# Kernel optimization log

Measured on AMD Instinct MI355X. Metric: run time of the kernel, lower is better.

## Reference

```python
import jax, jax.numpy as jnp
import numpy as np

C = 128          # inchannel
CH = C // 2      # projected channels
N_, D_, H_, W_ = 2, 16, 16, 16


def setup_inputs() -> dict:
    key = jax.random.key(0)
    kx, kq, kk, kv, kp = jax.random.split(key, 5)
    s_in = 1.0 / np.sqrt(C)
    s_mid = 1.0 / np.sqrt(CH)
    return {
        "x": jax.random.normal(kx, (N_, C, D_, H_, W_), dtype=jnp.float32),
        "Wq": jax.random.normal(kq, (CH, C), dtype=jnp.float32) * s_in,
        "Wk": jax.random.normal(kk, (CH, C), dtype=jnp.float32) * s_in,
        "Wv": jax.random.normal(kv, (CH, C), dtype=jnp.float32) * s_in,
        "Wpost": jax.random.normal(kp, (C, CH), dtype=jnp.float32) * s_mid,
    }


def reference(x, Wq, Wk, Wv, Wpost):
    n, c_in, d, h, w = x.shape
    npos = d * h * w
    xf = x.reshape(n, c_in, npos)                     # (n, C, N)
    # 1x1x1 conv3d (no bias) == channel-mixing matmul
    q = jnp.einsum('oc,ncx->nox', Wq, xf)             # (n, CH, N)
    k = jnp.einsum('oc,ncx->nox', Wk, xf)             # (n, CH, N)
    v = jnp.einsum('oc,ncx->nox', Wv, xf)             # (n, CH, N)
    # atten_map[b,i,j] = sum_c k[b,c,i] * q[b,c,j], softmax over j (dim=2)
    scores = jnp.einsum('nci,ncj->nij', k, q)         # (n, N, N)
    attn = jax.nn.softmax(scores, axis=2)
    # val @ attn: out[b,c,j] = sum_i v[b,c,i] * attn[b,i,j]
    agg = jnp.einsum('nci,nij->ncj', v, attn)         # (n, CH, N)
    post = jnp.einsum('oc,ncx->nox', Wpost, agg)      # (n, C, N)
    return post.reshape(n, c_in, d, h, w) + x
```

## Files before the change

kernel.cpp:

```cpp
#include <hip/hip_runtime.h>
#include <math.h>

#define NB   2
#define CIN  128
#define CH   64
#define NPOS 4096

typedef __attribute__((ext_vector_type(8))) short s16x8;
typedef __attribute__((ext_vector_type(4))) float f32x4;

__device__ __forceinline__ unsigned int bfrne(float f) {
    unsigned int u = __float_as_uint(f);
    return (u + 0x7FFFu + ((u >> 16) & 1u)) >> 16;
}
__device__ __forceinline__ unsigned int pk_rne(float lo, float hi) {
    return bfrne(lo) | (bfrne(hi) << 16);
}
__device__ __forceinline__ unsigned int pk_fast(float lo, float hi) {
    unsigned int a = (__float_as_uint(lo) + 0x8000u) >> 16;
    unsigned int b = (__float_as_uint(hi) + 0x8000u) & 0xFFFF0000u;
    return a | b;
}
__device__ __forceinline__ float bf2f(unsigned short h) {
    return __uint_as_float(((unsigned int)h) << 16);
}

#define XTS 132
__global__ __launch_bounds__(256) void qkv_kernel(
    const float* __restrict__ x,
    const float* __restrict__ Wq, const float* __restrict__ Wk,
    const float* __restrict__ Wv,
    unsigned short* __restrict__ kT, unsigned short* __restrict__ qT,
    unsigned short* __restrict__ vbs)
{
    __shared__ __align__(16) float xT[16 * XTS];
    const int b  = blockIdx.y;
    const int p0 = blockIdx.x * 16;
    const int tid = threadIdx.x;

    #pragma unroll
    for (int it = 0; it < 2; ++it) {
        int idx = it * 256 + tid;
        int c = idx >> 2, p4 = (idx & 3) * 4;
        float4 g = *(const float4*)&x[((size_t)b * CIN + c) * NPOS + p0 + p4];
        xT[(p4 + 0) * XTS + c] = g.x;
        xT[(p4 + 1) * XTS + c] = g.y;
        xT[(p4 + 2) * XTS + c] = g.z;
        xT[(p4 + 3) * XTS + c] = g.w;
    }
    __syncthreads();

    const int w = tid >> 6, l = tid & 63, lm = l & 15, lq = l >> 4;
    const int p = p0 + lm;

    s16x8 Bhi[4], Blo[4];
    #pragma unroll
    for (int ck = 0; ck < 4; ++ck) {
        const float* xr = &xT[lm * XTS + ck * 32 + lq * 8];
        union { unsigned int u[4]; s16x8 v; } chv, clv;
        #pragma unroll
        for (int j = 0; j < 4; ++j) {
            float x0 = xr[2 * j], x1 = xr[2 * j + 1];
            unsigned int h0 = bfrne(x0), h1 = bfrne(x1);
            chv.u[j] = h0 | (h1 << 16);
            clv.u[j] = pk_rne(x0 - __uint_as_float(h0 << 16),
                              x1 - __uint_as_float(h1 << 16));
        }
        Bhi[ck] = chv.v; Blo[ck] = clv.v;
    }

    #pragma unroll
    for (int t3 = 0; t3 < 3; ++t3) {
        const int tile = w * 3 + t3;
        const int mat = tile >> 2, o0 = (tile & 3) * 16;
        const float* __restrict__ W = (mat == 0) ? Wq : (mat == 1) ? Wk : Wv;
        f32x4 acc = {0.f, 0.f, 0.f, 0.f};
        #pragma unroll
        for (int ck = 0; ck < 4; ++ck) {
            const float* wp = W + (o0 + lm) * CIN + ck * 32 + lq * 8;
            union { unsigned int u[4]; s16x8 v; } ca;
            #pragma unroll
            for (int j = 0; j < 4; ++j) ca.u[j] = pk_rne(wp[2*j], wp[2*j+1]);
            acc = __builtin_amdgcn_mfma_f32_16x16x32_bf16(ca.v, Bhi[ck], acc, 0,0,0);
            acc = __builtin_amdgcn_mfma_f32_16x16x32_bf16(ca.v, Blo[ck], acc, 0,0,0);
        }
        if (mat < 2) {
            unsigned short* dst = (mat == 0) ? qT : kT;
            uint2 st = make_uint2(pk_rne(acc[0], acc[1]), pk_rne(acc[2], acc[3]));
            *(uint2*)&dst[((size_t)b * NPOS + p) * CH + o0 + lq * 4] = st;
        } else {
            #pragma unroll
            for (int r = 0; r < 4; ++r)
                vbs[((size_t)b * CH + o0 + lq * 4 + r) * NPOS + p] =
                    (unsigned short)bfrne(acc[r]);
        }
    }
}

__global__ __launch_bounds__(256, 4) void stats_kernel(
    const unsigned short* __restrict__ kT,
    const unsigned short* __restrict__ qT,
    float* __restrict__ lpart)
{
    __shared__ __align__(16) unsigned short qbuf[2][4096];
    const int b  = blockIdx.z;
    const int jq = blockIdx.y;
    const int i0 = blockIdx.x * 128;
    const int tid = threadIdx.x;
    const int w = tid >> 6, l = tid & 63, lm = l & 15, lq = l >> 4;

    s16x8 a[2][2];
    #pragma unroll
    for (int s = 0; s < 2; ++s)
        #pragma unroll
        for (int kc = 0; kc < 2; ++kc)
            a[s][kc] = *(const s16x8*)&kT[
                ((size_t)b * NPOS + i0 + w * 32 + s * 16 + lm) * CH + kc * 32 + lq * 8];

    const unsigned short* qpt =
        qT + ((size_t)b * NPOS + jq * 512 + w * 16 + lm) * CH + lq * 8;
    s16x8 st0 = *(const s16x8*)(qpt);
    s16x8 st1 = *(const s16x8*)(qpt + 32);

    float rs[2][4] = {};
    for (int t = 0; t < 8; ++t) {
        const int buf = t & 1;
        *(s16x8*)&qbuf[buf][(2 * w + 0) * 512 + l * 8] = st0;
        *(s16x8*)&qbuf[buf][(2 * w + 1) * 512 + l * 8] = st1;
        if (t < 7) {
            const unsigned short* qn = qpt + (size_t)(t + 1) * 64 * CH;
            st0 = *(const s16x8*)(qn);
            st1 = *(const s16x8*)(qn + 32);
        }
        __syncthreads();
        #pragma unroll
        for (int js = 0; js < 4; ++js) {
            s16x8 b0 = *(const s16x8*)&qbuf[buf][(js * 2 + 0) * 512 + l * 8];
            s16x8 b1 = *(const s16x8*)&qbuf[buf][(js * 2 + 1) * 512 + l * 8];
            #pragma unroll
            for (int s = 0; s < 2; ++s) {
                f32x4 sc = {0.f, 0.f, 0.f, 0.f};
                sc = __builtin_amdgcn_mfma_f32_16x16x32_bf16(a[s][0], b0, sc, 0,0,0);
                sc = __builtin_amdgcn_mfma_f32_16x16x32_bf16(a[s][1], b1, sc, 0,0,0);
                rs[s][0] += __expf(sc[0]); rs[s][1] += __expf(sc[1]);
                rs[s][2] += __expf(sc[2]); rs[s][3] += __expf(sc[3]);
            }
        }
    }

    #pragma unroll
    for (int s = 0; s < 2; ++s)
        #pragma unroll
        for (int r = 0; r < 4; ++r) {
            rs[s][r] += __shfl_xor(rs[s][r], 1);
            rs[s][r] += __shfl_xor(rs[s][r], 2);
            rs[s][r] += __shfl_xor(rs[s][r], 4);
            rs[s][r] += __shfl_xor(rs[s][r], 8);
        }
    if (lm == 0) {
        #pragma unroll
        for (int s = 0; s < 2; ++s)
            #pragma unroll
            for (int r = 0; r < 4; ++r)
                lpart[(size_t)jq * NB * NPOS + b * NPOS
                      + i0 + w * 32 + s * 16 + lq * 4 + r] = rs[s][r];
    }
}

__global__ __launch_bounds__(256, 4) void agg_kernel(
    const unsigned short* __restrict__ kT,
    const unsigned short* __restrict__ qT,
    const unsigned short* __restrict__ vbs,
    const float* __restrict__ lpart,
    unsigned short* __restrict__ U)
{
    __shared__ __align__(16) unsigned short kbuf[2][2048];
    __shared__ __align__(16) unsigned short vbuf[2][2048];
    __shared__ __align__(16) unsigned short wts[4][16][40];
    __shared__ __align__(16) float rls[512];
    const int b  = blockIdx.z;
    const int iq = blockIdx.y;
    const int j0 = blockIdx.x * 128;
    const int tid = threadIdx.x;
    const int w = tid >> 6, l = tid & 63, lm = l & 15, lq = l >> 4;

    {
        const float* lp = lpart + (size_t)b * NPOS + iq * 512 + tid * 2;
        float s0 = 0.f, s1 = 0.f;
        #pragma unroll
        for (int qq = 0; qq < 8; ++qq) {
            float2 lv = *(const float2*)(lp + (size_t)qq * NB * NPOS);
            s0 += lv.x; s1 += lv.y;
        }
        rls[tid * 2 + 0] = 1.0f / s0;
        rls[tid * 2 + 1] = 1.0f / s1;
    }

    s16x8 qb[2][2];
    #pragma unroll
    for (int js = 0; js < 2; ++js)
        #pragma unroll
        for (int kc = 0; kc < 2; ++kc)
            qb[js][kc] = *(const s16x8*)&qT[
                ((size_t)b * NPOS + j0 + w * 32 + js * 16 + lm) * CH + kc * 32 + lq * 8];

    const unsigned short* kpt = kT
        + ((size_t)b * NPOS + iq * 512 + (w >> 1) * 16 + lm) * CH
        + (w & 1) * 32 + lq * 8;
    const unsigned short* vpt = vbs
        + ((size_t)b * CH + w * 16 + lm) * NPOS + iq * 512 + lq * 8;

    f32x4 acc[2][4] = {};
    s16x8 kst = *(const s16x8*)kpt;
    s16x8 vst = *(const s16x8*)vpt;

    for (int t = 0; t < 16; ++t) {
        const int buf = t & 1;
        *(s16x8*)&kbuf[buf][w * 512 + l * 8] = kst;
        *(s16x8*)&vbuf[buf][w * 512 + l * 8] = vst;
        if (t < 15) {
            kst = *(const s16x8*)(kpt + (t + 1) * 32 * CH);
            vst = *(const s16x8*)(vpt + (t + 1) * 32);
        }
        __syncthreads();

        s16x8 kA[2][2], vA[4];
        #pragma unroll
        for (int s = 0; s < 2; ++s)
            #pragma unroll
            for (int kc = 0; kc < 2; ++kc)
                kA[s][kc] = *(const s16x8*)&kbuf[buf][(s * 2 + kc) * 512 + l * 8];
        #pragma unroll
        for (int cs = 0; cs < 4; ++cs)
            vA[cs] = *(const s16x8*)&vbuf[buf][cs * 512 + l * 8];

        f32x4 rl0 = *(const f32x4*)&rls[t * 32 + lq * 4];
        f32x4 rl1 = *(const f32x4*)&rls[t * 32 + 16 + lq * 4];

        #pragma unroll
        for (int js = 0; js < 2; ++js) {
            f32x4 s0 = {0,0,0,0}, s1 = {0,0,0,0};
            s0 = __builtin_amdgcn_mfma_f32_16x16x32_bf16(kA[0][0], qb[js][0], s0, 0,0,0);
            s0 = __builtin_amdgcn_mfma_f32_16x16x32_bf16(kA[0][1], qb[js][1], s0, 0,0,0);
            s1 = __builtin_amdgcn_mfma_f32_16x16x32_bf16(kA[1][0], qb[js][0], s1, 0,0,0);
            s1 = __builtin_amdgcn_mfma_f32_16x16x32_bf16(kA[1][1], qb[js][1], s1, 0,0,0);

            unsigned int P0[2], P1[2];
            P0[0] = pk_fast(__expf(s0[0]) * rl0[0], __expf(s0[1]) * rl0[1]);
            P0[1] = pk_fast(__expf(s0[2]) * rl0[2], __expf(s0[3]) * rl0[3]);
            P1[0] = pk_fast(__expf(s1[0]) * rl1[0], __expf(s1[1]) * rl1[1]);
            P1[1] = pk_fast(__expf(s1[2]) * rl1[2], __expf(s1[3]) * rl1[3]);

            *(uint2*)&wts[w][lm][4 * lq]      = make_uint2(P0[0], P0[1]);
            *(uint2*)&wts[w][lm][16 + 4 * lq] = make_uint2(P1[0], P1[1]);
            s16x8 Bv = *(const s16x8*)&wts[w][lm][8 * lq];

            #pragma unroll
            for (int cs = 0; cs < 4; ++cs)
                acc[js][cs] = __builtin_amdgcn_mfma_f32_16x16x32_bf16(
                    vA[cs], Bv, acc[js][cs], 0,0,0);
        }
    }

    unsigned short* Up = U + ((size_t)iq * NB + b) * NPOS * CH;
    #pragma unroll
    for (int js = 0; js < 2; ++js)
        #pragma unroll
        for (int cs = 0; cs < 4; ++cs) {
            uint2 st = make_uint2(pk_rne(acc[js][cs][0], acc[js][cs][1]),
                                  pk_rne(acc[js][cs][2], acc[js][cs][3]));
            *(uint2*)&Up[(size_t)(j0 + w * 32 + js * 16 + lm) * CH
                         + cs * 16 + lq * 4] = st;
        }
}

__global__ __launch_bounds__(256) void post_kernel(
    const float* __restrict__ x, const float* __restrict__ Wpost,
    const unsigned short* __restrict__ U, float* __restrict__ out)
{
    const int b  = blockIdx.y;
    const int p0 = blockIdx.x * 32;
    const int tid = threadIdx.x;
    const int w = tid >> 6, l = tid & 63, lm = l & 15, lq = l >> 4;
    const int psub = (w & 1) * 16, ohalf = w >> 1;
    const int p = p0 + psub + lm;
    const size_t PS = (size_t)NB * NPOS * CH;

    const unsigned short* u = U + ((size_t)b * NPOS + p) * CH;
    s16x8 Bf[2];
    #pragma unroll
    for (int ck = 0; ck < 2; ++ck) {
        float sv[8] = {};
        #pragma unroll
        for (int qq = 0; qq < 8; ++qq) {
            union { s16x8 v; unsigned short us[8]; } uu;
            uu.v = *(const s16x8*)(u + (size_t)qq * PS + ck * 32 + lq * 8);
            #pragma unroll
            for (int j = 0; j < 8; ++j) sv[j] += bf2f(uu.us[j]);
        }
        union { unsigned int u[4]; s16x8 v; } cb;
        #pragma unroll
        for (int j = 0; j < 4; ++j) cb.u[j] = pk_rne(sv[2*j], sv[2*j+1]);
        Bf[ck] = cb.v;
    }

    #pragma unroll
    for (int ot = 0; ot < 4; ++ot) {
        const int o0 = (ohalf * 4 + ot) * 16;
        f32x4 acc = {0.f, 0.f, 0.f, 0.f};
        #pragma unroll
        for (int ck = 0; ck < 2; ++ck) {
            const float* wp = Wpost + (o0 + lm) * CH + ck * 32 + lq * 8;
            union { unsigned int u[4]; s16x8 v; } ca;
            #pragma unroll
            for (int j = 0; j < 4; ++j) ca.u[j] = pk_rne(wp[2*j], wp[2*j+1]);
            acc = __builtin_amdgcn_mfma_f32_16x16x32_bf16(ca.v, Bf[ck], acc, 0,0,0);
        }
        #pragma unroll
        for (int r = 0; r < 4; ++r) {
            size_t gi = ((size_t)b * CIN + o0 + lq * 4 + r) * NPOS + p;
            out[gi] = x[gi] + acc[r];
        }
    }
}

extern "C" void kernel_launch(void* const* d_in, const int* in_sizes, int n_in,
                              void* d_out, int out_size, void* d_ws, size_t ws_size,
                              hipStream_t stream) {
    const float* x     = (const float*)d_in[0];
    const float* Wq    = (const float*)d_in[1];
    const float* Wk    = (const float*)d_in[2];
    const float* Wv    = (const float*)d_in[3];
    const float* Wpost = (const float*)d_in[4];
    float* out = (float*)d_out;

    unsigned short* kT  = (unsigned short*)d_ws;
    unsigned short* qT  = kT + (size_t)NB * NPOS * CH;
    unsigned short* vbs = qT + (size_t)NB * NPOS * CH;
    float* lpart = (float*)(vbs + (size_t)NB * NPOS * CH);
    unsigned short* U = (unsigned short*)(lpart + (size_t)8 * NB * NPOS);

    qkv_kernel  <<<dim3(NPOS / 16, NB),    256, 0, stream>>>(x, Wq, Wk, Wv, kT, qT, vbs);
    stats_kernel<<<dim3(NPOS / 128, 8, NB), 256, 0, stream>>>(kT, qT, lpart);
    agg_kernel  <<<dim3(NPOS / 128, 8, NB), 256, 0, stream>>>(kT, qT, vbs, lpart, U);
    post_kernel <<<dim3(NPOS / 32, NB),    256, 0, stream>>>(x, Wpost, U, out);
}
```

Measured before the change: 108.1 us.

## Store Q/K/V in MFMA fragment layout and load operands directly from global

The QKV projection now writes Q, K and V into a pre-swizzled fragment layout, so each lane's MFMA operand is one contiguous 16-byte chunk. The stats and aggregation kernels drop their LDS staging buffers and most __syncthreads, instead register-prefetching the next fragments straight from global memory (L2). The aim is to cut LDS traffic and barrier stalls. In exchange each wave issues more global loads, redundantly across waves, and agg's occupancy hint drops from 4 to 3 blocks.

```diff
diff --git a/kernel.cpp b/kernel.cpp
--- a/kernel.cpp
+++ b/kernel.cpp
@@ -8,6 +8,9 @@
 
 typedef __attribute__((ext_vector_type(8))) short s16x8;
 typedef __attribute__((ext_vector_type(4))) float f32x4;
+
+#define FB(b,T,kc) ((((size_t)(b) * 256 + (size_t)(T)) * 2 + (size_t)(kc)) * 512)
+#define VB(b,ct,it) ((((size_t)(b) * 4 + (size_t)(ct)) * 128 + (size_t)(it)) * 512)
 
 __device__ __forceinline__ unsigned int bfrne(float f) {
     unsigned int u = __float_as_uint(f);
@@ -30,12 +33,13 @@
     const float* __restrict__ x,
     const float* __restrict__ Wq, const float* __restrict__ Wk,
     const float* __restrict__ Wv,
-    unsigned short* __restrict__ kT, unsigned short* __restrict__ qT,
-    unsigned short* __restrict__ vbs)
+    unsigned short* __restrict__ kF, unsigned short* __restrict__ qF,
+    unsigned short* __restrict__ vF)
 {
     __shared__ __align__(16) float xT[16 * XTS];
     const int b  = blockIdx.y;
-    const int p0 = blockIdx.x * 16;
+    const int pt = blockIdx.x;
+    const int p0 = pt * 16;
     const int tid = threadIdx.x;
 
     #pragma unroll
@@ -51,7 +55,6 @@
     __syncthreads();
 
     const int w = tid >> 6, l = tid & 63, lm = l & 15, lq = l >> 4;
-    const int p = p0 + lm;
 
     s16x8 Bhi[4], Blo[4];
     #pragma unroll
@@ -85,66 +88,59 @@
             acc = __builtin_amdgcn_mfma_f32_16x16x32_bf16(ca.v, Blo[ck], acc, 0,0,0);
         }
         if (mat < 2) {
-            unsigned short* dst = (mat == 0) ? qT : kT;
+            unsigned short* dst = (mat == 0) ? qF : kF;
+            const int kc = o0 >> 5;
+            const int lane2 = lm + 16 * (((o0 & 31) >> 3) + (lq >> 1));
             uint2 st = make_uint2(pk_rne(acc[0], acc[1]), pk_rne(acc[2], acc[3]));
-            *(uint2*)&dst[((size_t)b * NPOS + p) * CH + o0 + lq * 4] = st;
+            *(uint2*)&dst[FB(b, pt, kc) + lane2 * 8 + (lq & 1) * 4] = st;
         } else {
+            const int ct = o0 >> 4;
+            const int itile = pt >> 1;
+            const int lanebase = 16 * ((pt & 1) * 2 + (lm >> 3));
             #pragma unroll
             for (int r = 0; r < 4; ++r)
-                vbs[((size_t)b * CH + o0 + lq * 4 + r) * NPOS + p] =
-                    (unsigned short)bfrne(acc[r]);
+                vF[VB(b, ct, itile) + (size_t)(4 * lq + r + lanebase) * 8
+                   + (lm & 7)] = (unsigned short)bfrne(acc[r]);
         }
     }
 }
 
 __global__ __launch_bounds__(256, 4) void stats_kernel(
-    const unsigned short* __restrict__ kT,
-    const unsigned short* __restrict__ qT,
+    const unsigned short* __restrict__ kF,
+    const unsigned short* __restrict__ qF,
     float* __restrict__ lpart)
 {
-    __shared__ __align__(16) unsigned short qbuf[2][4096];
     const int b  = blockIdx.z;
     const int jq = blockIdx.y;
-    const int i0 = blockIdx.x * 128;
     const int tid = threadIdx.x;
     const int w = tid >> 6, l = tid & 63, lm = l & 15, lq = l >> 4;
+    const int it = blockIdx.x * 4 + w;
 
     s16x8 a[2][2];
     #pragma unroll
     for (int s = 0; s < 2; ++s)
         #pragma unroll
         for (int kc = 0; kc < 2; ++kc)
-            a[s][kc] = *(const s16x8*)&kT[
-                ((size_t)b * NPOS + i0 + w * 32 + s * 16 + lm) * CH + kc * 32 + lq * 8];
-
-    const unsigned short* qpt =
-        qT + ((size_t)b * NPOS + jq * 512 + w * 16 + lm) * CH + lq * 8;
-    s16x8 st0 = *(const s16x8*)(qpt);
-    s16x8 st1 = *(const s16x8*)(qpt + 32);
+            a[s][kc] = *(const s16x8*)&kF[FB(b, it * 2 + s, kc) + l * 8];
+
+    const unsigned short* q0 = qF + FB(b, jq * 32, 0);
+    s16x8 nb0 = *(const s16x8*)&q0[l * 8];
+    s16x8 nb1 = *(const s16x8*)&q0[512 + l * 8];
 
     float rs[2][4] = {};
-    for (int t = 0; t < 8; ++t) {
-        const int buf = t & 1;
-        *(s16x8*)&qbuf[buf][(2 * w + 0) * 512 + l * 8] = st0;
-        *(s16x8*)&qbuf[buf][(2 * w + 1) * 512 + l * 8] = st1;
-        if (t < 7) {
-            const unsigned short* qn = qpt + (size_t)(t + 1) * 64 * CH;
-            st0 = *(const s16x8*)(qn);
-            st1 = *(const s16x8*)(qn + 32);
-        }
-        __syncthreads();
-        #pragma unroll
-        for (int js = 0; js < 4; ++js) {
-            s16x8 b0 = *(const s16x8*)&qbuf[buf][(js * 2 + 0) * 512 + l * 8];
-            s16x8 b1 = *(const s16x8*)&qbuf[buf][(js * 2 + 1) * 512 + l * 8];
-            #pragma unroll
-            for (int s = 0; s < 2; ++s) {
-                f32x4 sc = {0.f, 0.f, 0.f, 0.f};
-                sc = __builtin_amdgcn_mfma_f32_16x16x32_bf16(a[s][0], b0, sc, 0,0,0);
-                sc = __builtin_amdgcn_mfma_f32_16x16x32_bf16(a[s][1], b1, sc, 0,0,0);
-                rs[s][0] += __expf(sc[0]); rs[s][1] += __expf(sc[1]);
-                rs[s][2] += __expf(sc[2]); rs[s][3] += __expf(sc[3]);
-            }
+    for (int t = 0; t < 32; ++t) {
+        s16x8 b0 = nb0, b1 = nb1;
+        if (t < 31) {
+            nb0 = *(const s16x8*)&q0[(size_t)(t + 1) * 1024 + l * 8];
+            nb1 = *(const s16x8*)&q0[(size_t)(t + 1) * 1024 + 512 + l * 8];
+        }
+        #pragma unroll
+        for (int s = 0; s < 2; ++s) {
+            f32x4 sc = {0.f, 0.f, 0.f, 0.f};
+            sc = __builtin_amdgcn_mfma_f32_16x16x32_bf16(a[s][0], b0, sc, 0,0,0);
+            sc = __builtin_amdgcn_mfma_f32_16x16x32_bf16(a[s][1], b1, sc, 0,0,0);
+            rs[s][0] += __expf(sc[0]); rs[s][1] += __expf(sc[1]);
+            rs[s][2] += __expf(sc[2]); rs[s][3] += __expf(sc[3]);
         }
     }
 
@@ -163,19 +159,17 @@
             #pragma unroll
             for (int r = 0; r < 4; ++r)
                 lpart[(size_t)jq * NB * NPOS + b * NPOS
-                      + i0 + w * 32 + s * 16 + lq * 4 + r] = rs[s][r];
-    }
-}
-
-__global__ __launch_bounds__(256, 4) void agg_kernel(
-    const unsigned short* __restrict__ kT,
-    const unsigned short* __restrict__ qT,
-    const unsigned short* __restrict__ vbs,
+                      + it * 32 + s * 16 + lq * 4 + r] = rs[s][r];
+    }
+}
+
+__global__ __launch_bounds__(256, 3) void agg_kernel(
+    const unsigned short* __restrict__ kF,
+    const unsigned short* __restrict__ qF,
+    const unsigned short* __restrict__ vF,
     const float* __restrict__ lpart,
     unsigned short* __restrict__ U)
 {
-    __shared__ __align__(16) unsigned short kbuf[2][2048];
-    __shared__ __align__(16) unsigned short vbuf[2][2048];
     __shared__ __align__(16) unsigned short wts[4][16][40];
     __shared__ __align__(16) float rls[512];
     const int b  = blockIdx.z;
@@ -201,38 +195,36 @@
     for (int js = 0; js < 2; ++js)
         #pragma unroll
         for (int kc = 0; kc < 2; ++kc)
-            qb[js][kc] = *(const s16x8*)&qT[
-                ((size_t)b * NPOS + j0 + w * 32 + js * 16 + lm) * CH + kc * 32 + lq * 8];
-
-    const unsigned short* kpt = kT
-        + ((size_t)b * NPOS + iq * 512 + (w >> 1) * 16 + lm) * CH
-        + (w & 1) * 32 + lq * 8;
-    const unsigned short* vpt = vbs
-        + ((size_t)b * CH + w * 16 + lm) * NPOS + iq * 512 + lq * 8;
+            qb[js][kc] = *(const s16x8*)&qF[
+                FB(b, blockIdx.x * 8 + w * 2 + js, kc) + l * 8];
 
     f32x4 acc[2][4] = {};
-    s16x8 kst = *(const s16x8*)kpt;
-    s16x8 vst = *(const s16x8*)vpt;
+    s16x8 nk[2][2], nv[4];
+    #pragma unroll
+    for (int s = 0; s < 2; ++s)
+        #pragma unroll
+        for (int kc = 0; kc < 2; ++kc)
+            nk[s][kc] = *(const s16x8*)&kF[FB(b, iq * 32 + s, kc) + l * 8];
+    #pragma unroll
+    for (int cs = 0; cs < 4; ++cs)
+        nv[cs] = *(const s16x8*)&vF[VB(b, cs, iq * 16) + l * 8];
+
+    __syncthreads();
 
     for (int t = 0; t < 16; ++t) {
-        const int buf = t & 1;
-        *(s16x8*)&kbuf[buf][w * 512 + l * 8] = kst;
-        *(s16x8*)&vbuf[buf][w * 512 + l * 8] = vst;
+        s16x8 kA[2][2] = {{nk[0][0], nk[0][1]}, {nk[1][0], nk[1][1]}};
+        s16x8 vA[4] = {nv[0], nv[1], nv[2], nv[3]};
         if (t < 15) {
-            kst = *(const s16x8*)(kpt + (t + 1) * 32 * CH);
-            vst = *(const s16x8*)(vpt + (t + 1) * 32);
-        }
-        __syncthreads();
-
-        s16x8 kA[2][2], vA[4];
-        #pragma unroll
-        for (int s = 0; s < 2; ++s)
-            #pragma unroll
-            for (int kc = 0; kc < 2; ++kc)
-                kA[s][kc] = *(const s16x8*)&kbuf[buf][(s * 2 + kc) * 512 + l * 8];
-        #pragma unroll
-        for (int cs = 0; cs < 4; ++cs)
-            vA[cs] = *(const s16x8*)&vbuf[buf][cs * 512 + l * 8];
+            #pragma unroll
+            for (int s = 0; s < 2; ++s)
+                #pragma unroll
+                for (int kc = 0; kc < 2; ++kc)
+                    nk[s][kc] = *(const s16x8*)&kF[
+                        FB(b, iq * 32 + (t + 1) * 2 + s, kc) + l * 8];
+            #pragma unroll
+            for (int cs = 0; cs < 4; ++cs)
+                nv[cs] = *(const s16x8*)&vF[VB(b, cs, iq * 16 + t + 1) + l * 8];
+        }
 
         f32x4 rl0 = *(const f32x4*)&rls[t * 32 + lq * 4];
         f32x4 rl1 = *(const f32x4*)&rls[t * 32 + 16 + lq * 4];
@@ -334,14 +326,14 @@
     const float* Wpost = (const float*)d_in[4];
     float* out = (float*)d_out;
 
-    unsigned short* kT  = (unsigned short*)d_ws;
-    unsigned short* qT  = kT + (size_t)NB * NPOS * CH;
-    unsigned short* vbs = qT + (size_t)NB * NPOS * CH;
-    float* lpart = (float*)(vbs + (size_t)NB * NPOS * CH);
+    unsigned short* kF = (unsigned short*)d_ws;
+    unsigned short* qF = kF + (size_t)NB * NPOS * CH;
+    unsigned short* vF = qF + (size_t)NB * NPOS * CH;
+    float* lpart = (float*)(vF + (size_t)NB * NPOS * CH);
     unsigned short* U = (unsigned short*)(lpart + (size_t)8 * NB * NPOS);
 
-    qkv_kernel  <<<dim3(NPOS / 16, NB),    256, 0, stream>>>(x, Wq, Wk, Wv, kT, qT, vbs);
-    stats_kernel<<<dim3(NPOS / 128, 8, NB), 256, 0, stream>>>(kT, qT, lpart);
-    agg_kernel  <<<dim3(NPOS / 128, 8, NB), 256, 0, stream>>>(kT, qT, vbs, lpart, U);
-    post_kernel <<<dim3(NPOS / 32, NB),    256, 0, stream>>>(x, Wpost, U, out);
-}
+    qkv_kernel  <<<dim3(NPOS / 16, NB),     256, 0, stream>>>(x, Wq, Wk, Wv, kF, qF, vF);
+    stats_kernel<<<dim3(32, 8, NB),         256, 0, stream>>>(kF, qF, lpart);
+    agg_kernel  <<<dim3(NPOS / 128, 8, NB), 256, 0, stream>>>(kF, qF, vF, lpart, U);
+    post_kernel <<<dim3(NPOS / 32, NB),     256, 0, stream>>>(x, Wpost, U, out);
+}
```

After: 104.2 us. -3.7%, faster.
